# Optimization experiments

Measured on AMD Instinct MI355X. Metric: run time of the kernel, lower is better.

The kernel has to match this reference:

```python
import jax, jax.numpy as jnp
import numpy as np

N, H, C, K, D = 16384, 16, 192, 43, 2
SIGMA = 1.0   # radius == sigma in Block
BN_EPS = 1e-5


def setup_inputs() -> dict:
    key = jax.random.key(0)
    ks = jax.random.split(key, 8)
    coord = jax.random.uniform(ks[0], (N, 3), dtype=jnp.float32)
    feat = jax.random.normal(ks[1], (N, C), dtype=jnp.float32)
    ref_idx = jax.random.randint(ks[2], (N, H), 0, N)
    # kernel point dispositions, within radius
    kp = jax.random.normal(ks[3], (K, 3), dtype=jnp.float32) * (0.3 * SIGMA)
    W1 = jax.random.normal(ks[4], (D, C, C), dtype=jnp.float32) / np.sqrt(C)
    Wk = jax.random.normal(ks[5], (D, K, C), dtype=jnp.float32) / np.sqrt(K * H)
    W3 = jax.random.normal(ks[6], (D, C, C), dtype=jnp.float32) / np.sqrt(C)
    ones = jnp.ones((D, C), jnp.float32)
    zeros = jnp.zeros((D, C), jnp.float32)
    return {
        "coord": coord, "feat": feat, "ref_idx": ref_idx, "kp": kp,
        "W1": W1, "Wk": Wk, "W3": W3,
        "g1": ones, "b1": zeros, "g2": ones, "b2": zeros, "g3": ones, "b3": zeros,
    }


def _bn(x, g, b):
    # PointBatchNorm on [N, C]: batch statistics over the point axis
    m = jnp.mean(x, axis=0)
    v = jnp.var(x, axis=0)
    return (x - m) * jax.lax.rsqrt(v + BN_EPS) * g + b


def reference(coord, feat, ref_idx, kp, W1, Wk, W3, g1, b1, g2, b2, g3, b3):
    # --- KP influence, shared across blocks (same coords / neighbor table) ---
    nb = coord[ref_idx] - coord[:, None, :]                       # [N,H,3] relative neighbor coords
    d2 = (jnp.sum(nb * nb, -1)[..., None]
          + jnp.sum(kp * kp, -1)[None, None, :]
          - 2.0 * jnp.einsum('nhd,kd->nhk', nb, kp))              # [N,H,K]
    d = jnp.sqrt(jnp.maximum(d2, 0.0))
    infl = jnp.maximum(1.0 - d / SIGMA, 0.0)                      # linear influence [N,H,K]

    relu = jax.nn.relu
    depth = W1.shape[0]
    for i in range(depth):
        identity = feat
        h = relu(_bn(feat @ W1[i], g1[i], b1[i]))                 # fc1 + BN + ReLU
        # KPConvD: depthwise kernel-point conv
        A = jnp.einsum('nhk,kc->nhc', infl, Wk[i])                # influence-projected depthwise weights
        h = jnp.einsum('nhc,nhc->nc', h[ref_idx], A)              # gather + weighted aggregate
        h = relu(_bn(h, g2[i], b2[i]))
        h = _bn(h @ W3[i], g3[i], b3[i])                          # fc3 + BN
        feat = relu(identity + h)                                 # skip + ReLU
    return feat
```

## Files before the change

### kernel.cpp

```cpp
#include <hip/hip_runtime.h>

#define N_PTS 16384
#define NH 16
#define NC 192
#define NK 43
#define ND 2
#define BN_EPS 1e-5f

typedef __attribute__((ext_vector_type(8))) short bf16x8;
typedef __attribute__((ext_vector_type(4))) float f32x4;

static __device__ __forceinline__ short f2bf(float f) {
    union { float f; unsigned u; } x; x.f = f;
    unsigned r = x.u + (0x7fffu + ((x.u >> 16) & 1u));
    return (short)(r >> 16);
}
static __device__ __forceinline__ float bf2f(short s) {
    union { unsigned u; float f; } x; x.u = ((unsigned)(unsigned short)s) << 16;
    return x.f;
}

__global__ __launch_bounds__(64) void k_wfrag(const float* __restrict__ W1,
                                              const float* __restrict__ Wk,
                                              const float* __restrict__ W3,
                                              short* __restrict__ Wb) {
    int b = blockIdx.x;
    int d = b / 168, r = b % 168;
    const float* src; short* dst; int kb, Ks, tile;
    if (r < 72)      { src = W1 + d * NC * NC; dst = Wb + d * 86016;         kb = 6; Ks = NC; tile = r; }
    else if (r < 96) { src = Wk + d * NK * NC; dst = Wb + d * 86016 + 36864; kb = 2; Ks = NK; tile = r - 72; }
    else             { src = W3 + d * NC * NC; dst = Wb + d * 86016 + 49152; kb = 6; Ks = NC; tile = r - 96; }
    int nt = tile / kb, ks = tile % kb;
    int lane = threadIdx.x, quad = lane >> 4, cl = lane & 15;
    bf16x8 vv;
#pragma unroll
    for (int j = 0; j < 8; ++j) {
        int k = ks * 32 + quad * 8 + j;
        vv[j] = (k < Ks) ? f2bf(src[k * NC + nt * 16 + cl]) : (short)0;
    }
    *(bf16x8*)(dst + ((nt * kb + ks) * 64 + lane) * 8) = vv;
}

__global__ __launch_bounds__(128) void k_stat2(const float* __restrict__ part, int nb,
                                               const float* __restrict__ g,
                                               const float* __restrict__ b,
                                               float* __restrict__ a_out,
                                               float* __restrict__ s_out) {
    __shared__ float red2[2];
    const int c = blockIdx.x;
    const int tid = threadIdx.x;
    const int lane = tid & 63;
    const int half = tid >> 6;
    const float* src = part + (half ? 192 + c : c);
    float s = 0.f;
    for (int i = lane; i < nb; i += 64) s += src[i * 384];
    s += __shfl_xor(s, 1);  s += __shfl_xor(s, 2);  s += __shfl_xor(s, 4);
    s += __shfl_xor(s, 8);  s += __shfl_xor(s, 16); s += __shfl_xor(s, 32);
    if (lane == 0) red2[half] = s;
    __syncthreads();
    if (tid == 0) {
        float m = red2[0] * (1.f / N_PTS);
        float var = red2[1] * (1.f / N_PTS) - m * m;
        float rs = rsqrtf(var + BN_EPS);
        float a = rs * g[c];
        a_out[c] = a;
        s_out[c] = b[c] - m * a;
    }
}

__global__ __launch_bounds__(192) void k_stat1b(const short* __restrict__ A,
                                                float* __restrict__ part) {
    __shared__ float red[8][384];
    const int tid = threadIdx.x;
    const int g = tid / 24, m = tid % 24;
    float s8[8], q8[8];
#pragma unroll
    for (int j = 0; j < 8; ++j) { s8[j] = 0.f; q8[j] = 0.f; }
#pragma unroll
    for (int p = 0; p < 4; ++p) {
        int row = blockIdx.x * 32 + p * 8 + g;
        bf16x8 v = *(const bf16x8*)(A + row * NC + m * 8);
#pragma unroll
        for (int j = 0; j < 8; ++j) {
            float x = bf2f(v[j]);
            s8[j] += x; q8[j] = fmaf(x, x, q8[j]);
        }
    }
#pragma unroll
    for (int j = 0; j < 8; ++j) {
        red[g][m * 8 + j] = s8[j];
        red[g][192 + m * 8 + j] = q8[j];
    }
    __syncthreads();
    float S = 0.f, Q = 0.f;
#pragma unroll
    for (int gg = 0; gg < 8; ++gg) { S += red[gg][tid]; Q += red[gg][192 + tid]; }
    part[blockIdx.x * 384 + tid] = S;
    part[blockIdx.x * 384 + 192 + tid] = Q;
}

__global__ __launch_bounds__(256) void k_gemm1(const float* __restrict__ feat,
                                               const short* __restrict__ T2prev,
                                               const float* __restrict__ st3prev,
                                               short* __restrict__ X1,
                                               const short* __restrict__ W1b,
                                               short* __restrict__ T,
                                               float* __restrict__ part) {
    __shared__ float red[4][384];
    const int tid = threadIdx.x;
    const int wave = tid >> 6, lane = tid & 63;
    const int quad = lane >> 4, cl = lane & 15;
    const int r0 = blockIdx.x * 64 + wave * 16;
    const int row = r0 + cl;

    f32x4 acc[12];
#pragma unroll
    for (int nt = 0; nt < 12; ++nt) acc[nt] = (f32x4){0.f, 0.f, 0.f, 0.f};

#pragma unroll
    for (int ks = 0; ks < 6; ++ks) {
        const int k0 = ks * 32 + quad * 8;
        const float* ap = feat + row * NC + k0;
        float4 a0 = *(const float4*)ap;
        float4 a1v = *(const float4*)(ap + 4);
        float x[8] = {a0.x, a0.y, a0.z, a0.w, a1v.x, a1v.y, a1v.z, a1v.w};
        if (T2prev) {
            bf16x8 t2 = *(const bf16x8*)(T2prev + row * NC + k0);
            float4 pa0 = *(const float4*)(st3prev + k0), pa1 = *(const float4*)(st3prev + k0 + 4);
            float4 ps0 = *(const float4*)(st3prev + 192 + k0), ps1 = *(const float4*)(st3prev + 192 + k0 + 4);
            float pav[8] = {pa0.x, pa0.y, pa0.z, pa0.w, pa1.x, pa1.y, pa1.z, pa1.w};
            float psv[8] = {ps0.x, ps0.y, ps0.z, ps0.w, ps1.x, ps1.y, ps1.z, ps1.w};
#pragma unroll
            for (int j = 0; j < 8; ++j)
                x[j] = fmaxf(x[j] + fmaf(pav[j], bf2f(t2[j]), psv[j]), 0.f);
        }
        bf16x8 af;
#pragma unroll
        for (int j = 0; j < 8; ++j) af[j] = f2bf(x[j]);
        if (T2prev) *(bf16x8*)(X1 + row * NC + k0) = af;
#pragma unroll
        for (int nt = 0; nt < 12; ++nt) {
            bf16x8 bf = *(const bf16x8*)(W1b + ((nt * 6 + ks) * 64 + lane) * 8);
            acc[nt] = __builtin_amdgcn_mfma_f32_16x16x32_bf16(af, bf, acc[nt], 0, 0, 0);
        }
    }
#pragma unroll
    for (int nt = 0; nt < 12; ++nt) {
        int c = nt * 16 + cl;
        float s = 0.f, sq = 0.f;
#pragma unroll
        for (int r = 0; r < 4; ++r) {
            float v = acc[nt][r];
            T[(r0 + quad * 4 + r) * NC + c] = f2bf(v);
            s += v; sq = fmaf(v, v, sq);
        }
        s += __shfl_xor(s, 16); s += __shfl_xor(s, 32);
        sq += __shfl_xor(sq, 16); sq += __shfl_xor(sq, 32);
        if (quad == 0) { red[wave][c] = s; red[wave][192 + c] = sq; }
    }
    __syncthreads();
    for (int t = tid; t < 384; t += 256)
        part[blockIdx.x * 384 + t] = red[0][t] + red[1][t] + red[2][t] + red[3][t];
}

__global__ __launch_bounds__(512) void k_kpconv(const float* __restrict__ coord,
                                                const int* __restrict__ ridx,
                                                const float* __restrict__ kp,
                                                const short* __restrict__ Wkb,
                                                const short* __restrict__ T,
                                                const float* __restrict__ st1,
                                                short* __restrict__ U) {
    __shared__ __align__(16) short wk_s[12288];
    __shared__ __align__(16) float4 kp_s[64];
    __shared__ float a1s[192], s1s[192];
    __shared__ __align__(16) unsigned short gbuf[8 * 16 * 200];

    const int tid = threadIdx.x;
    {
        const float4* src = (const float4*)Wkb;
        float4* dst = (float4*)wk_s;
        for (int j = tid; j < 1536; j += 512) dst[j] = src[j];
        if (tid < 64) {
            bool ok = tid < NK;
            float x = ok ? kp[tid * 3 + 0] : 1e9f;
            float y = ok ? kp[tid * 3 + 1] : 1e9f;
            float z = ok ? kp[tid * 3 + 2] : 1e9f;
            kp_s[tid] = (float4){x, y, z, fmaf(x, x, fmaf(y, y, z * z))};
        }
        if (tid < 192) { a1s[tid] = st1[tid]; s1s[tid] = st1[192 + tid]; }
    }
    __syncthreads();

    const int wave = tid >> 6, lane = tid & 63;
    const int quad = lane >> 4, cl = lane & 15;
    const int n = blockIdx.x * 8 + wave;

    int idh = 0; float nbx = 0.f, nby = 0.f, nbz = 0.f;
    if (lane < NH) {
        idh = ridx[n * NH + lane];
        float cx = coord[n * 3 + 0], cy = coord[n * 3 + 1], cz = coord[n * 3 + 2];
        nbx = coord[idh * 3 + 0] - cx;
        nby = coord[idh * 3 + 1] - cy;
        nbz = coord[idh * 3 + 2] - cz;
    }
    const float nx = __shfl(nbx, cl), ny = __shfl(nby, cl), nz = __shfl(nbz, cl);

    unsigned short* gw = gbuf + wave * 3200;
    const unsigned short* Tu = (const unsigned short*)T;
#pragma unroll
    for (int i = 0; i < 6; ++i) {
        int g = i * 64 + lane;
        int row = g / 24, seg = g - row * 24;
        int gr = __shfl(idh, row);
        uint4 v = *(const uint4*)(Tu + gr * NC + seg * 8);
        *(uint4*)(gw + row * 200 + seg * 8) = v;
    }

    const float nb2 = fmaf(nx, nx, fmaf(ny, ny, nz * nz));
    const float m2x = -2.f * nx, m2y = -2.f * ny, m2z = -2.f * nz;
    bf16x8 af[2];
#pragma unroll
    for (int ks = 0; ks < 2; ++ks) {
#pragma unroll
        for (int j = 0; j < 8; ++j) {
            int k = ks * 32 + quad * 8 + j;
            float4 kpv = kp_s[k];
            float t = nb2 + kpv.w;
            t = fmaf(m2x, kpv.x, t);
            t = fmaf(m2y, kpv.y, t);
            t = fmaf(m2z, kpv.z, t);
            float d = sqrtf(fmaxf(t, 0.f));
            af[ks][j] = f2bf(fmaxf(1.f - d, 0.f));
        }
    }

    f32x4 acc[12];
#pragma unroll
    for (int nt = 0; nt < 12; ++nt) {
        bf16x8 b0 = *(const bf16x8*)(wk_s + ((nt * 2 + 0) * 64 + lane) * 8);
        bf16x8 b1v = *(const bf16x8*)(wk_s + ((nt * 2 + 1) * 64 + lane) * 8);
        f32x4 z = (f32x4){0.f, 0.f, 0.f, 0.f};
        z = __builtin_amdgcn_mfma_f32_16x16x32_bf16(af[0], b0, z, 0, 0, 0);
        acc[nt] = __builtin_amdgcn_mfma_f32_16x16x32_bf16(af[1], b1v, z, 0, 0, 0);
    }

#pragma unroll
    for (int nt = 0; nt < 12; ++nt) {
        const float a1c = a1s[nt * 16 + cl], s1c = s1s[nt * 16 + cl];
        float u = 0.f;
#pragma unroll
        for (int r = 0; r < 4; ++r) {
            unsigned short tv = gw[(quad * 4 + r) * 200 + nt * 16 + cl];
            float t = bf2f((short)tv);
            float x = fmaxf(fmaf(a1c, t, s1c), 0.f);
            u = fmaf(acc[nt][r], x, u);
        }
        u += __shfl_xor(u, 16);
        u += __shfl_xor(u, 32);
        if (quad == 0) U[n * NC + nt * 16 + cl] = f2bf(u);
    }
}

__global__ __launch_bounds__(256) void k_gemm3(const short* __restrict__ U,
                                               const float* __restrict__ st2,
                                               const short* __restrict__ W3b,
                                               short* __restrict__ T2,
                                               float* __restrict__ part) {
    __shared__ float red[4][384];
    const int tid = threadIdx.x;
    const int wave = tid >> 6, lane = tid & 63;
    const int quad = lane >> 4, cl = lane & 15;
    const int r0 = blockIdx.x * 64 + wave * 16;
    const int row = r0 + cl;

    f32x4 acc[12];
#pragma unroll
    for (int nt = 0; nt < 12; ++nt) acc[nt] = (f32x4){0.f, 0.f, 0.f, 0.f};

#pragma unroll
    for (int ks = 0; ks < 6; ++ks) {
        const int k0 = ks * 32 + quad * 8;
        bf16x8 u8 = *(const bf16x8*)(U + row * NC + k0);
        float4 aa0 = *(const float4*)(st2 + k0), aa1 = *(const float4*)(st2 + k0 + 4);
        float4 ss0 = *(const float4*)(st2 + 192 + k0), ss1 = *(const float4*)(st2 + 192 + k0 + 4);
        float av[8] = {aa0.x, aa0.y, aa0.z, aa0.w, aa1.x, aa1.y, aa1.z, aa1.w};
        float sv[8] = {ss0.x, ss0.y, ss0.z, ss0.w, ss1.x, ss1.y, ss1.z, ss1.w};
        bf16x8 af;
#pragma unroll
        for (int j = 0; j < 8; ++j)
            af[j] = f2bf(fmaxf(fmaf(av[j], bf2f(u8[j]), sv[j]), 0.f));
#pragma unroll
        for (int nt = 0; nt < 12; ++nt) {
            bf16x8 bf = *(const bf16x8*)(W3b + ((nt * 6 + ks) * 64 + lane) * 8);
            acc[nt] = __builtin_amdgcn_mfma_f32_16x16x32_bf16(af, bf, acc[nt], 0, 0, 0);
        }
    }
#pragma unroll
    for (int nt = 0; nt < 12; ++nt) {
        int c = nt * 16 + cl;
        float s = 0.f, sq = 0.f;
#pragma unroll
        for (int r = 0; r < 4; ++r) {
            float v = acc[nt][r];
            T2[(r0 + quad * 4 + r) * NC + c] = f2bf(v);
            s += v; sq = fmaf(v, v, sq);
        }
        s += __shfl_xor(s, 16); s += __shfl_xor(s, 32);
        sq += __shfl_xor(sq, 16); sq += __shfl_xor(sq, 32);
        if (quad == 0) { red[wave][c] = s; red[wave][192 + c] = sq; }
    }
    __syncthreads();
    for (int t = tid; t < 384; t += 256)
        part[blockIdx.x * 384 + t] = red[0][t] + red[1][t] + red[2][t] + red[3][t];
}

__global__ __launch_bounds__(256) void k_final(const short* __restrict__ T2,
                                               const float* __restrict__ st3,
                                               const short* __restrict__ X1,
                                               float* __restrict__ out) {
    const int i = blockIdx.x * 256 + threadIdx.x;
    const int c0 = (i * 8) % 192;
    bf16x8 t2 = *(const bf16x8*)(T2 + (long)i * 8);
    bf16x8 x1 = *(const bf16x8*)(X1 + (long)i * 8);
    float4 aa0 = *(const float4*)(st3 + c0), aa1 = *(const float4*)(st3 + c0 + 4);
    float4 ss0 = *(const float4*)(st3 + 192 + c0), ss1 = *(const float4*)(st3 + 192 + c0 + 4);
    float av[8] = {aa0.x, aa0.y, aa0.z, aa0.w, aa1.x, aa1.y, aa1.z, aa1.w};
    float sv[8] = {ss0.x, ss0.y, ss0.z, ss0.w, ss1.x, ss1.y, ss1.z, ss1.w};
    float o[8];
#pragma unroll
    for (int j = 0; j < 8; ++j)
        o[j] = fmaxf(bf2f(x1[j]) + fmaf(av[j], bf2f(t2[j]), sv[j]), 0.f);
    *(float4*)(out + (long)i * 8)     = (float4){o[0], o[1], o[2], o[3]};
    *(float4*)(out + (long)i * 8 + 4) = (float4){o[4], o[5], o[6], o[7]};
}

extern "C" void kernel_launch(void* const* d_in, const int* in_sizes, int n_in,
                              void* d_out, int out_size, void* d_ws, size_t ws_size,
                              hipStream_t stream) {
    const float* coord = (const float*)d_in[0];
    const float* feat  = (const float*)d_in[1];
    const int*   ridx  = (const int*)d_in[2];
    const float* kp    = (const float*)d_in[3];
    const float* W1    = (const float*)d_in[4];
    const float* Wk    = (const float*)d_in[5];
    const float* W3    = (const float*)d_in[6];
    const float* g1    = (const float*)d_in[7];
    const float* b1    = (const float*)d_in[8];
    const float* g2    = (const float*)d_in[9];
    const float* b2    = (const float*)d_in[10];
    const float* g3    = (const float*)d_in[11];
    const float* b3    = (const float*)d_in[12];
    float* out = (float*)d_out;

    float* part  = (float*)d_ws;
    float* stats = part + 512 * 384;
    short* X1 = (short*)(stats + 2304);
    short* T  = X1 + N_PTS * NC;
    short* U  = T + N_PTS * NC;
    short* T2 = U + N_PTS * NC;
    short* Wb = T2 + N_PTS * NC;

    k_wfrag<<<336, 64, 0, stream>>>(W1, Wk, W3, Wb);

    for (int d = 0; d < ND; ++d) {
        const short* W1b = Wb + d * 86016;
        const short* Wkb = W1b + 36864;
        const short* W3b = W1b + 49152;
        float* st1 = stats + (d * 3 + 0) * 384;
        float* st2 = stats + (d * 3 + 1) * 384;
        float* st3 = stats + (d * 3 + 2) * 384;

        k_gemm1<<<256, 256, 0, stream>>>(feat,
                                         d ? T2 : (short*)nullptr,
                                         stats + 2 * 384,
                                         X1, W1b, T, part);
        k_stat2<<<192, 128, 0, stream>>>(part, 256, g1 + d * NC, b1 + d * NC, st1, st1 + 192);
        k_kpconv<<<N_PTS / 8, 512, 0, stream>>>(coord, ridx, kp, Wkb, T, st1, U);
        k_stat1b<<<512, 192, 0, stream>>>(U, part);
        k_stat2<<<192, 128, 0, stream>>>(part, 512, g2 + d * NC, b2 + d * NC, st2, st2 + 192);
        k_gemm3<<<256, 256, 0, stream>>>(U, st2, W3b, T2, part);
        k_stat2<<<192, 128, 0, stream>>>(part, 256, g3 + d * NC, b3 + d * NC, st3, st3 + 192);
    }
    k_final<<<N_PTS * NC / 8 / 256, 256, 0, stream>>>(T2, stats + 5 * 384, X1, out);
}
```

Before: 265.7 us.

## Pre-convert features to bf16 and double points per kpconv block

The weight-fragment kernel now also converts the fp32 input features to bf16 in one extra pass. Both gemm1 launches then read the half-width bf16 copy, which removes the fp32 loads and conversions from the GEMM. The kpconv kernel now uses 1024 threads and 16 points per block, so the shared kernel-weight and kernel-point staging is spread over twice as many points. The trade-offs are that the residual input loses precision by being rounded to bf16 before the add, and kpconv needs much more LDS per block, which may cap it at one block per CU.

```diff
diff --git a/kernel.cpp b/kernel.cpp
--- a/kernel.cpp
+++ b/kernel.cpp
@@ -23,8 +23,20 @@
 __global__ __launch_bounds__(64) void k_wfrag(const float* __restrict__ W1,
                                               const float* __restrict__ Wk,
                                               const float* __restrict__ W3,
-                                              short* __restrict__ Wb) {
+                                              const float* __restrict__ feat,
+                                              short* __restrict__ Wb,
+                                              short* __restrict__ Fb) {
     int b = blockIdx.x;
+    if (b >= 336) {
+        long i = (long)(b - 336) * 512 + (long)threadIdx.x * 8;
+        float4 f0 = *(const float4*)(feat + i);
+        float4 f1 = *(const float4*)(feat + i + 4);
+        bf16x8 v;
+        v[0] = f2bf(f0.x); v[1] = f2bf(f0.y); v[2] = f2bf(f0.z); v[3] = f2bf(f0.w);
+        v[4] = f2bf(f1.x); v[5] = f2bf(f1.y); v[6] = f2bf(f1.z); v[7] = f2bf(f1.w);
+        *(bf16x8*)(Fb + i) = v;
+        return;
+    }
     int d = b / 168, r = b % 168;
     const float* src; short* dst; int kb, Ks, tile;
     if (r < 72)      { src = W1 + d * NC * NC; dst = Wb + d * 86016;         kb = 6; Ks = NC; tile = r; }
@@ -99,7 +111,7 @@
     part[blockIdx.x * 384 + 192 + tid] = Q;
 }
 
-__global__ __launch_bounds__(256) void k_gemm1(const float* __restrict__ feat,
+__global__ __launch_bounds__(256) void k_gemm1(const short* __restrict__ featb,
                                                const short* __restrict__ T2prev,
                                                const float* __restrict__ st3prev,
                                                short* __restrict__ X1,
@@ -120,10 +132,8 @@
 #pragma unroll
     for (int ks = 0; ks < 6; ++ks) {
         const int k0 = ks * 32 + quad * 8;
-        const float* ap = feat + row * NC + k0;
-        float4 a0 = *(const float4*)ap;
-        float4 a1v = *(const float4*)(ap + 4);
-        float x[8] = {a0.x, a0.y, a0.z, a0.w, a1v.x, a1v.y, a1v.z, a1v.w};
+        bf16x8 f8 = *(const bf16x8*)(featb + row * NC + k0);
+        bf16x8 af;
         if (T2prev) {
             bf16x8 t2 = *(const bf16x8*)(T2prev + row * NC + k0);
             float4 pa0 = *(const float4*)(st3prev + k0), pa1 = *(const float4*)(st3prev + k0 + 4);
@@ -132,12 +142,11 @@
             float psv[8] = {ps0.x, ps0.y, ps0.z, ps0.w, ps1.x, ps1.y, ps1.z, ps1.w};
 #pragma unroll
             for (int j = 0; j < 8; ++j)
-                x[j] = fmaxf(x[j] + fmaf(pav[j], bf2f(t2[j]), psv[j]), 0.f);
-        }
-        bf16x8 af;
-#pragma unroll
-        for (int j = 0; j < 8; ++j) af[j] = f2bf(x[j]);
-        if (T2prev) *(bf16x8*)(X1 + row * NC + k0) = af;
+                af[j] = f2bf(fmaxf(bf2f(f8[j]) + fmaf(pav[j], bf2f(t2[j]), psv[j]), 0.f));
+            *(bf16x8*)(X1 + row * NC + k0) = af;
+        } else {
+            af = f8;
+        }
 #pragma unroll
         for (int nt = 0; nt < 12; ++nt) {
             bf16x8 bf = *(const bf16x8*)(W1b + ((nt * 6 + ks) * 64 + lane) * 8);
@@ -163,23 +172,23 @@
         part[blockIdx.x * 384 + t] = red[0][t] + red[1][t] + red[2][t] + red[3][t];
 }
 
-__global__ __launch_bounds__(512) void k_kpconv(const float* __restrict__ coord,
-                                                const int* __restrict__ ridx,
-                                                const float* __restrict__ kp,
-                                                const short* __restrict__ Wkb,
-                                                const short* __restrict__ T,
-                                                const float* __restrict__ st1,
-                                                short* __restrict__ U) {
+__global__ __launch_bounds__(1024) void k_kpconv(const float* __restrict__ coord,
+                                                 const int* __restrict__ ridx,
+                                                 const float* __restrict__ kp,
+                                                 const short* __restrict__ Wkb,
+                                                 const short* __restrict__ T,
+                                                 const float* __restrict__ st1,
+                                                 short* __restrict__ U) {
     __shared__ __align__(16) short wk_s[12288];
     __shared__ __align__(16) float4 kp_s[64];
     __shared__ float a1s[192], s1s[192];
-    __shared__ __align__(16) unsigned short gbuf[8 * 16 * 200];
+    __shared__ __align__(16) unsigned short gbuf[16 * 16 * 200];
 
     const int tid = threadIdx.x;
     {
         const float4* src = (const float4*)Wkb;
         float4* dst = (float4*)wk_s;
-        for (int j = tid; j < 1536; j += 512) dst[j] = src[j];
+        for (int j = tid; j < 1536; j += 1024) dst[j] = src[j];
         if (tid < 64) {
             bool ok = tid < NK;
             float x = ok ? kp[tid * 3 + 0] : 1e9f;
@@ -193,7 +202,7 @@
 
     const int wave = tid >> 6, lane = tid & 63;
     const int quad = lane >> 4, cl = lane & 15;
-    const int n = blockIdx.x * 8 + wave;
+    const int n = blockIdx.x * 16 + wave;
 
     int idh = 0; float nbx = 0.f, nby = 0.f, nbz = 0.f;
     if (lane < NH) {
@@ -359,8 +368,9 @@
     short* U  = T + N_PTS * NC;
     short* T2 = U + N_PTS * NC;
     short* Wb = T2 + N_PTS * NC;
-
-    k_wfrag<<<336, 64, 0, stream>>>(W1, Wk, W3, Wb);
+    short* Fb = Wb + 2 * 86016;
+
+    k_wfrag<<<336 + 6144, 64, 0, stream>>>(W1, Wk, W3, feat, Wb, Fb);
 
     for (int d = 0; d < ND; ++d) {
         const short* W1b = Wb + d * 86016;
@@ -370,12 +380,12 @@
         float* st2 = stats + (d * 3 + 1) * 384;
         float* st3 = stats + (d * 3 + 2) * 384;
 
-        k_gemm1<<<256, 256, 0, stream>>>(feat,
+        k_gemm1<<<256, 256, 0, stream>>>(Fb,
                                          d ? T2 : (short*)nullptr,
                                          stats + 2 * 384,
                                          X1, W1b, T, part);
         k_stat2<<<192, 128, 0, stream>>>(part, 256, g1 + d * NC, b1 + d * NC, st1, st1 + 192);
-        k_kpconv<<<N_PTS / 8, 512, 0, stream>>>(coord, ridx, kp, Wkb, T, st1, U);
+        k_kpconv<<<N_PTS / 16, 1024, 0, stream>>>(coord, ridx, kp, Wkb, T, st1, U);
         k_stat1b<<<512, 192, 0, stream>>>(U, part);
         k_stat2<<<192, 128, 0, stream>>>(part, 512, g2 + d * NC, b2 + d * NC, st2, st2 + 192);
         k_gemm3<<<256, 256, 0, stream>>>(U, st2, W3b, T2, part);
```

New measurement: 275.6 us. +3.8%, slower.
